# Kernel tuning notes

Measured on AMD Instinct MI355X. Metric: run time of the kernel, lower is better.

Reference implementation:

```python
import jax, jax.numpy as jnp
import numpy as np

NUM_USER = 24000
NUM_ITEM = 8000
DIM_E = 64
V_DIM = 2048
T_DIM = 384
TOPK = 10
N_UI_LAYERS = 2
LAMBDA = 0.9
N_INTER = 400000


def _build_sim(x):
    xn = x / jnp.linalg.norm(x, axis=-1, keepdims=True)
    return xn @ xn.T


def _knn_sym(sim, topk):
    # top-k per row -> sparse graph with symmetric (D^-1/2 A D^-1/2) normalization
    n = sim.shape[0]
    val, ind = jax.lax.top_k(sim, topk)            # [n, k]
    row = jnp.repeat(jnp.arange(n), topk)
    w = val.reshape(-1)
    col = ind.reshape(-1)
    deg = jax.ops.segment_sum(w, row, num_segments=n)
    dis = jnp.where(deg > 0, deg ** -0.5, 0.0)     # inf -> 0 as in torch masked_fill
    return col, dis[row] * w * dis[col]


def setup_inputs() -> dict:
    key = jax.random.key(0)
    ks = jax.random.split(key, 12)
    user_emb = jax.random.normal(ks[0], (NUM_USER, DIM_E), jnp.float32) * 0.1
    item_emb = jax.random.normal(ks[1], (NUM_ITEM, DIM_E), jnp.float32) * 0.1
    v_feat = jax.random.normal(ks[2], (NUM_ITEM, V_DIM), jnp.float32)
    t_feat = jax.random.normal(ks[3], (NUM_ITEM, T_DIM), jnp.float32)
    W_v = jax.random.normal(ks[4], (V_DIM, DIM_E), jnp.float32) * (1.0 / np.sqrt(V_DIM))
    b_v = jnp.zeros((DIM_E,), jnp.float32)
    W_t = jax.random.normal(ks[5], (T_DIM, DIM_E), jnp.float32) * (1.0 / np.sqrt(T_DIM))
    b_t = jnp.zeros((DIM_E,), jnp.float32)
    Wq1 = jax.random.normal(ks[6], (DIM_E, DIM_E), jnp.float32) * (1.0 / np.sqrt(DIM_E))
    bq1 = jnp.zeros((DIM_E,), jnp.float32)
    wq2 = jax.random.normal(ks[7], (DIM_E,), jnp.float32) * (1.0 / np.sqrt(DIM_E))
    # bipartite user-item interaction edges, symmetrized (as in __init__)
    u = jax.random.randint(ks[8], (N_INTER,), 0, NUM_USER)
    it = jax.random.randint(ks[9], (N_INTER,), 0, NUM_ITEM) + NUM_USER
    ei = jnp.stack([u, it])
    edge_index = jnp.concatenate([ei, ei[::-1]], axis=1)  # [2, 2*N_INTER]
    # original (frozen) multimodal KNN graphs built from raw features at init
    orig_img_cols, orig_img_w = _knn_sym(_build_sim(v_feat), TOPK)
    orig_txt_cols, orig_txt_w = _knn_sym(_build_sim(t_feat), TOPK)
    return {"user_emb": user_emb, "item_emb": item_emb, "v_feat": v_feat,
            "t_feat": t_feat, "W_v": W_v, "b_v": b_v, "W_t": W_t, "b_t": b_t,
            "Wq1": Wq1, "bq1": bq1, "wq2": wq2,
            "orig_img_w": orig_img_w, "orig_txt_w": orig_txt_w,
            "edge_index": edge_index,
            "orig_img_cols": orig_img_cols, "orig_txt_cols": orig_txt_cols}


def reference(user_emb, item_emb, v_feat, t_feat, W_v, b_v, W_t, b_t,
              Wq1, bq1, wq2, orig_img_w, orig_txt_w,
              edge_index, orig_img_cols, orig_txt_cols):
    n_user, n_item = user_emb.shape[0], item_emb.shape[0]
    # modality projections
    image_feats = v_feat @ W_v + b_v
    text_feats = t_feat @ W_t + b_t
    # fresh KNN graphs from projected features (build_item_graph=True path)
    img_cols, img_w = _knn_sym(_build_sim(image_feats), TOPK)
    txt_cols, txt_w = _knn_sym(_build_sim(text_feats), TOPK)
    row = jnp.repeat(jnp.arange(n_item), TOPK)

    def fused_spmm(cols_new, w_new, cols_orig, w_orig, x):
        # (1-lam)*A_new + lam*A_orig, applied as a single sparse matmul
        rows = jnp.concatenate([row, row])
        cols = jnp.concatenate([cols_new, cols_orig])
        w = jnp.concatenate([(1.0 - LAMBDA) * w_new,
                             LAMBDA * jax.lax.stop_gradient(w_orig)])
        return jax.ops.segment_sum(w[:, None] * x[cols], rows, num_segments=n_item)

    # NOTE: source bug reproduced - mm_layers loop always re-reads item_embedding,
    # so effective propagation depth is 1 regardless of mm_layers.
    image_item = fused_spmm(img_cols, img_w, orig_img_cols, orig_img_w, item_emb)
    text_item = fused_spmm(txt_cols, txt_w, orig_txt_cols, orig_txt_w, item_emb)

    def q(x):
        return jnp.tanh(x @ Wq1 + bq1) @ wq2  # [n_item]

    att = jnp.stack([q(image_item), q(text_item)], axis=-1)  # [n_item, 2]
    wgt = jax.nn.softmax(att, axis=-1)
    h = wgt[:, :1] * image_item + wgt[:, 1:] * text_item

    # user-item GCN propagation with sym degree normalization
    ego = jnp.concatenate([user_emb, item_emb], axis=0)
    n = ego.shape[0]
    r, c = edge_index[0], edge_index[1]
    deg = jax.ops.segment_sum(jnp.ones_like(r, dtype=ego.dtype), r, num_segments=n)
    dis = jnp.where(deg > 0, deg ** -0.5, 0.0)
    norm = dis[r] * dis[c]
    embs = [ego]
    for _ in range(N_UI_LAYERS):
        ego = jax.ops.segment_sum(norm[:, None] * ego[c], r, num_segments=n)
        embs.append(ego)
    all_emb = jnp.mean(jnp.stack(embs, axis=1), axis=1)
    u_g, i_g = all_emb[:n_user], all_emb[n_user:]
    h_norm = h / jnp.maximum(jnp.linalg.norm(h, axis=1, keepdims=True), 1e-12)
    i_g = i_g + h_norm
    return jnp.concatenate([u_g, i_g], axis=0)
```

## Files before the change

kernel.cpp:

```cpp
#include <hip/hip_runtime.h>
#include <math.h>

#define N_USER 24000
#define N_ITEM 8000
#define N_NODE 32000
#define N_EDGE 800000
#define NJC    16
#define JCH    512

typedef __attribute__((ext_vector_type(8))) short bf16x8;
typedef __attribute__((ext_vector_type(4))) float f32x4;

__device__ __forceinline__ float wred_sum(float v) {
#pragma unroll
  for (int off = 32; off; off >>= 1) v += __shfl_xor(v, off, 64);
  return v;
}

__device__ __forceinline__ unsigned short f2bf(float f) {
  unsigned int u = __float_as_uint(f);
  unsigned int r = (u + 0x7fffu + ((u >> 16) & 1u)) >> 16;
  return (unsigned short)r;
}
__device__ __forceinline__ float bf2f(unsigned short h) {
  return __uint_as_float(((unsigned int)h) << 16);
}

__device__ __forceinline__ unsigned int umx(unsigned int a, unsigned int b) { return a > b ? a : b; }
__device__ __forceinline__ unsigned int umn(unsigned int a, unsigned int b) { return a < b ? a : b; }

__device__ __forceinline__ float key_val(unsigned int k) {
  return ((float)(int)(k >> 13) - 131080.0f) * (1.0f / 131072.0f);
}
__device__ __forceinline__ int key_idx(unsigned int k) {
  return 8191 - (int)(k & 8191u);
}

#define ASTR 132
__global__ __launch_bounds__(256) void gemm_dual(
    const float* __restrict__ Xi, const float* __restrict__ Wi,
    const float* __restrict__ Xt, const float* __restrict__ Wt,
    float* __restrict__ Pi, float* __restrict__ Pt)
{
  __shared__ float As[32 * ASTR];
  __shared__ float Bs[32 * 64];
  const int tid = threadIdx.x;
  const int m0 = blockIdx.x * 128;
  const int cy = blockIdx.y;
  const float* X; const float* W; float* out; int K, kc0, Klen;
  if (cy < 8) { X = Xi; W = Wi; K = 2048; Klen = 256; kc0 = cy * 256;
                out = Pi + (size_t)cy * N_ITEM * 64; }
  else        { X = Xt; W = Wt; K = 384;  Klen = 128; kc0 = (cy - 8) * 128;
                out = Pt + (size_t)(cy - 8) * N_ITEM * 64; }
  const int tr = tid >> 4, tc = tid & 15;
  float acc[8][4] = {};
  for (int k0 = kc0; k0 < kc0 + Klen; k0 += 32) {
    __syncthreads();
#pragma unroll
    for (int lq = 0; lq < 4; ++lq) {
      int u = tid + lq * 256;
      int r = u >> 3, kq = u & 7;
      int row = m0 + r; if (row > N_ITEM - 1) row = N_ITEM - 1;
      float4 a = *(const float4*)(X + (size_t)row * K + k0 + kq * 4);
      As[(kq * 4 + 0) * ASTR + r] = a.x;
      As[(kq * 4 + 1) * ASTR + r] = a.y;
      As[(kq * 4 + 2) * ASTR + r] = a.z;
      As[(kq * 4 + 3) * ASTR + r] = a.w;
    }
#pragma unroll
    for (int lq = 0; lq < 2; ++lq) {
      int u = tid + lq * 256;
      int kb = u >> 4, nq = u & 15;
      *(float4*)(Bs + kb * 64 + nq * 4) =
          *(const float4*)(W + (size_t)(k0 + kb) * 64 + nq * 4);
    }
    __syncthreads();
#pragma unroll
    for (int k = 0; k < 32; ++k) {
      float4 a0 = *(const float4*)(As + k * ASTR + tr * 8);
      float4 a1 = *(const float4*)(As + k * ASTR + tr * 8 + 4);
      float4 b4 = *(const float4*)(Bs + k * 64 + tc * 4);
      float av[8] = {a0.x, a0.y, a0.z, a0.w, a1.x, a1.y, a1.z, a1.w};
      float bv[4] = {b4.x, b4.y, b4.z, b4.w};
#pragma unroll
      for (int ri = 0; ri < 8; ++ri)
#pragma unroll
        for (int ci = 0; ci < 4; ++ci) acc[ri][ci] += av[ri] * bv[ci];
    }
  }
#pragma unroll
  for (int ri = 0; ri < 8; ++ri) {
    int row = m0 + tr * 8 + ri;
    if (row < N_ITEM) {
      float4 o;
      o.x = acc[ri][0]; o.y = acc[ri][1]; o.z = acc[ri][2]; o.w = acc[ri][3];
      *(float4*)(out + (size_t)row * 64 + tc * 4) = o;
    }
  }
}

__global__ __launch_bounds__(256) void norm_dual(
    const float* __restrict__ Pi, const float* __restrict__ bi,
    unsigned short* __restrict__ Xhi, unsigned short* __restrict__ Xli,
    const float* __restrict__ Pt, const float* __restrict__ bt,
    unsigned short* __restrict__ Xht, unsigned short* __restrict__ Xlt)
{
  const float* P; const float* bias; unsigned short *Xh, *Xl; int nk;
  if (blockIdx.y == 0) { P = Pi; bias = bi; Xh = Xhi; Xl = Xli; nk = 8; }
  else                 { P = Pt; bias = bt; Xh = Xht; Xl = Xlt; nk = 3; }
  int row = blockIdx.x * 4 + (threadIdx.x >> 6);
  int lane = threadIdx.x & 63;
  size_t o = (size_t)row * 64 + lane;
  float v = bias[lane];
  for (int q = 0; q < nk; ++q) v += P[(size_t)q * N_ITEM * 64 + o];
  float ss = wred_sum(v * v);
  float xn = v * rsqrtf(ss);
  unsigned short hi = f2bf(xn);
  Xh[o] = hi;
  Xl[o] = f2bf(xn - bf2f(hi));
}

__global__ __launch_bounds__(256) void sim_topk_mfma(
    const unsigned short* __restrict__ Xhi, const unsigned short* __restrict__ Xli,
    const unsigned short* __restrict__ Xht, const unsigned short* __restrict__ Xlt,
    unsigned int* __restrict__ pk)
{
  __shared__ char lds[2 * 2 * 32 * 128];
  const unsigned short* Xh = blockIdx.z ? Xht : Xhi;
  const unsigned short* Xl = blockIdx.z ? Xlt : Xli;
  unsigned int* pkm = pk + (size_t)blockIdx.z * N_ITEM * (NJC * 10);

  const int tid = threadIdx.x;
  const int l = tid & 63;
  const int wid = tid >> 6;
  const int ib = blockIdx.x * 128 + wid * 32;
  const int jc = blockIdx.y * JCH;
  const bool lastc = (jc + JCH > N_ITEM);

  bf16x8 bh[2][2], bl[2][2];
#pragma unroll
  for (int s = 0; s < 2; ++s) {
    int irow = ib + s * 16 + (l & 15);
    if (irow > N_ITEM - 1) irow = N_ITEM - 1;
    int ksl = (l >> 4) * 8;
#pragma unroll
    for (int kh = 0; kh < 2; ++kh) {
      bh[s][kh] = *(const bf16x8*)(Xh + (size_t)irow * 64 + kh * 32 + ksl);
      bl[s][kh] = *(const bf16x8*)(Xl + (size_t)irow * 64 + kh * 32 + ksl);
    }
  }

  unsigned int K0[10], K1[10];
#pragma unroll
  for (int t = 0; t < 10; ++t) { K0[t] = 0u; K1[t] = 0u; }

  auto stage = [&](int b, int p) {
    int row = tid >> 3, cb = (tid & 7) * 16;
    int gr = jc + p * 32 + row;
    if (gr > N_ITEM - 1) gr = N_ITEM - 1;
    int4 vh = *(const int4*)(Xh + (size_t)gr * 64 + (cb >> 1));
    int4 vl = *(const int4*)(Xl + (size_t)gr * 64 + (cb >> 1));
    int bo = (row * 128 + cb) ^ ((row & 7) << 4);
    *(int4*)(lds + b * 8192 + bo) = vh;
    *(int4*)(lds + b * 8192 + 4096 + bo) = vl;
  };

#define EPI(MASKED)                                                            \
  _Pragma("unroll")                                                            \
  for (int s = 0; s < 2; ++s) {                                                \
    unsigned int* K = s ? K1 : K0;                                             \
    _Pragma("unroll")                                                          \
    for (int t = 0; t < 2; ++t) {                                              \
      _Pragma("unroll")                                                        \
      for (int r = 0; r < 4; ++r) {                                            \
        float f = acc[t][s][r];                                                \
        unsigned int v19 = (unsigned int)(int)(f * 131072.0f + 131080.0f);     \
        unsigned int key = (v19 << 13) | (unsigned int)jinv[t * 4 + r];        \
        if (MASKED) key = (jinv[t * 4 + r] >= 192) ? key : 0u;                 \
        _Pragma("unroll")                                                      \
        for (int q = 0; q < 10; ++q) {                                         \
          unsigned int mn = umn(K[q], key);                                    \
          K[q] = umx(K[q], key);                                               \
          key = mn;                                                            \
        }                                                                      \
      }                                                                        \
    }                                                                          \
  }

  stage(0, 0);
  int cur = 0;
  for (int p = 0; p < 16; ++p) {
    __syncthreads();
    if (p < 15) stage(cur ^ 1, p + 1);
    const char* ldsH = lds + cur * 8192;
    const char* ldsL = ldsH + 4096;
    f32x4 acc[2][2] = {};
#pragma unroll
    for (int t = 0; t < 2; ++t) {
      int jr = t * 16 + (l & 15);
      int sw = (jr & 7) << 4;
      int rb = jr * 128 + ((l >> 4) << 4);
      bf16x8 ah0 = *(const bf16x8*)(ldsH + (rb ^ sw));
      bf16x8 ah1 = *(const bf16x8*)(ldsH + ((rb + 64) ^ sw));
      bf16x8 al0 = *(const bf16x8*)(ldsL + (rb ^ sw));
      bf16x8 al1 = *(const bf16x8*)(ldsL + ((rb + 64) ^ sw));
#pragma unroll
      for (int s = 0; s < 2; ++s) {
        acc[t][s] = __builtin_amdgcn_mfma_f32_16x16x32_bf16(ah0, bh[s][0], acc[t][s], 0, 0, 0);
        acc[t][s] = __builtin_amdgcn_mfma_f32_16x16x32_bf16(ah1, bh[s][1], acc[t][s], 0, 0, 0);
        acc[t][s] = __builtin_amdgcn_mfma_f32_16x16x32_bf16(ah0, bl[s][0], acc[t][s], 0, 0, 0);
        acc[t][s] = __builtin_amdgcn_mfma_f32_16x16x32_bf16(ah1, bl[s][1], acc[t][s], 0, 0, 0);
        acc[t][s] = __builtin_amdgcn_mfma_f32_16x16x32_bf16(al0, bh[s][0], acc[t][s], 0, 0, 0);
        acc[t][s] = __builtin_amdgcn_mfma_f32_16x16x32_bf16(al1, bh[s][1], acc[t][s], 0, 0, 0);
      }
    }
    const int jg0 = jc + p * 32 + ((l >> 4) << 2);
    int jinv[8];
#pragma unroll
    for (int t = 0; t < 2; ++t)
#pragma unroll
      for (int r = 0; r < 4; ++r)
        jinv[t * 4 + r] = 8191 - (jg0 + t * 16 + r);
    if (!lastc) { EPI(false) } else { EPI(true) }
    cur ^= 1;
  }
#undef EPI

#pragma unroll
  for (int s = 0; s < 2; ++s) {
    unsigned int* K = s ? K1 : K0;
    unsigned int kv[10];
#pragma unroll
    for (int t = 0; t < 10; ++t) {
      unsigned int m = K[0];
      m = umx(m, (unsigned int)__shfl_xor((int)m, 16, 64));
      m = umx(m, (unsigned int)__shfl_xor((int)m, 32, 64));
      bool own = (K[0] == m);
#pragma unroll
      for (int q2 = 0; q2 < 9; ++q2) K[q2] = own ? K[q2 + 1] : K[q2];
      K[9] = own ? 0u : K[9];
      kv[t] = m;
    }
    int i = ib + s * 16 + (l & 15);
    if (l < 16 && i < N_ITEM) {
      size_t base = ((size_t)i * NJC + blockIdx.y) * 10;
#pragma unroll
      for (int t = 0; t < 10; ++t) pkm[base + t] = kv[t];
    }
  }
}

__global__ __launch_bounds__(256) void merge_topk(
    const unsigned int* __restrict__ pk,
    float* __restrict__ tv_i, int* __restrict__ tc_i, float* __restrict__ dis_i,
    float* __restrict__ tv_t, int* __restrict__ tc_t, float* __restrict__ dis_t)
{
  float* tv; int* tc; float* dis;
  if (blockIdx.y == 0) { tv = tv_i; tc = tc_i; dis = dis_i; }
  else                 { tv = tv_t; tc = tc_t; dis = dis_t; }
  int lane = threadIdx.x & 63;
  int row = blockIdx.x * 4 + (threadIdx.x >> 6);
  size_t base = (size_t)blockIdx.y * N_ITEM * (NJC * 10) + (size_t)row * (NJC * 10);
  unsigned int k0 = pk[base + lane];
  unsigned int k1 = pk[base + 64 + lane];
  unsigned int k2 = (lane < 32) ? pk[base + 128 + lane] : 0u;
  float deg = 0.f, keepv = 0.f; int keepc = 0;
  for (int t = 0; t < 10; ++t) {
    unsigned int m = umx(umx(k0, k1), k2);
#pragma unroll
    for (int off = 32; off; off >>= 1)
      m = umx(m, (unsigned int)__shfl_xor((int)m, off, 64));
    deg += key_val(m);
    if (k0 == m) k0 = 0u;
    else if (k1 == m) k1 = 0u;
    else if (k2 == m) k2 = 0u;
    if (lane == t) { keepv = key_val(m); keepc = key_idx(m); }
  }
  if (lane < 10) { tv[(size_t)row * 10 + lane] = keepv; tc[(size_t)row * 10 + lane] = keepc; }
  if (lane == 0) dis[row] = deg > 0.f ? rsqrtf(deg) : 0.f;
}

__global__ __launch_bounds__(256) void spmm_attn(
    const float* __restrict__ tv_i, const int* __restrict__ tc_i, const float* __restrict__ dis_i,
    const float* __restrict__ ow_i, const int* __restrict__ oc_i,
    const float* __restrict__ tv_t, const int* __restrict__ tc_t, const float* __restrict__ dis_t,
    const float* __restrict__ ow_t, const int* __restrict__ oc_t,
    const float* __restrict__ item_emb,
    const float* __restrict__ Wq1, const float* __restrict__ bq1,
    const float* __restrict__ wq2, float* __restrict__ hn)
{
  __shared__ float Wlds[64 * 64];
  __shared__ float sm[4][2][64];
  int tid = threadIdx.x;
  int lane = tid & 63, wid = tid >> 6;
  int row = blockIdx.x * 4 + wid;
#pragma unroll
  for (int s = 0; s < 4; ++s) {
    int idx = tid + s * 256;
    ((float4*)Wlds)[idx] = ((const float4*)Wq1)[idx];
  }
  float a0 = 0.f, a1 = 0.f;
  {
    float disr = dis_i[row];
#pragma unroll
    for (int t = 0; t < 10; ++t) {
      int c = tc_i[(size_t)row * 10 + t];
      a0 += 0.1f * disr * tv_i[(size_t)row * 10 + t] * dis_i[c] * item_emb[(size_t)c * 64 + lane];
    }
#pragma unroll
    for (int t = 0; t < 10; ++t) {
      int c = oc_i[(size_t)row * 10 + t];
      a0 += 0.9f * ow_i[(size_t)row * 10 + t] * item_emb[(size_t)c * 64 + lane];
    }
  }
  {
    float disr = dis_t[row];
#pragma unroll
    for (int t = 0; t < 10; ++t) {
      int c = tc_t[(size_t)row * 10 + t];
      a1 += 0.1f * disr * tv_t[(size_t)row * 10 + t] * dis_t[c] * item_emb[(size_t)c * 64 + lane];
    }
#pragma unroll
    for (int t = 0; t < 10; ++t) {
      int c = oc_t[(size_t)row * 10 + t];
      a1 += 0.9f * ow_t[(size_t)row * 10 + t] * item_emb[(size_t)c * 64 + lane];
    }
  }
  sm[wid][0][lane] = a0;
  sm[wid][1][lane] = a1;
  __syncthreads();
  float y0 = bq1[lane], y1 = bq1[lane];
  for (int k = 0; k < 64; ++k) {
    float w = Wlds[k * 64 + lane];
    y0 += sm[wid][0][k] * w;
    y1 += sm[wid][1][k] * w;
  }
  float wq = wq2[lane];
  float s0 = wred_sum(tanhf(y0) * wq);
  float s1 = wred_sum(tanhf(y1) * wq);
  float mx = fmaxf(s0, s1);
  float e0 = expf(s0 - mx), e1 = expf(s1 - mx);
  float inv = 1.f / (e0 + e1);
  float h = (e0 * inv) * a0 + (e1 * inv) * a1;
  float n2 = wred_sum(h * h);
  float nrm = fmaxf(sqrtf(n2), 1e-12f);
  hn[(size_t)row * 64 + lane] = h / nrm;
}

__global__ void ui_zero(int* degi, int* cursor)
{
  int n = blockIdx.x * 256 + threadIdx.x;
  if (n < N_NODE) { degi[n] = 0; cursor[n] = 0; }
}

__global__ void ui_count(const int* __restrict__ r, int* degi)
{
  int e = blockIdx.x * 256 + threadIdx.x;
  if (e < N_EDGE) atomicAdd(&degi[r[e]], 1);
}

__global__ __launch_bounds__(256) void ui_blocksum(const int* __restrict__ degi, int* __restrict__ bsum)
{
  __shared__ int ws4[4];
  int tid = threadIdx.x;
  int v = degi[blockIdx.x * 256 + tid];
#pragma unroll
  for (int off = 32; off; off >>= 1) v += __shfl_xor(v, off, 64);
  if ((tid & 63) == 0) ws4[tid >> 6] = v;
  __syncthreads();
  if (tid == 0) bsum[blockIdx.x] = ws4[0] + ws4[1] + ws4[2] + ws4[3];
}

__global__ __launch_bounds__(128) void ui_scanb(const int* __restrict__ bsum, int* __restrict__ bbase, int* __restrict__ offs)
{
  __shared__ int s[128];
  int t = threadIdx.x;
  int v = (t < 125) ? bsum[t] : 0;
  s[t] = v;
  __syncthreads();
  for (int off = 1; off < 128; off <<= 1) {
    int tmp = (t >= off) ? s[t - off] : 0;
    __syncthreads();
    s[t] += tmp;
    __syncthreads();
  }
  if (t < 125) bbase[t] = s[t] - v;
  if (t == 127) offs[N_NODE] = s[127];
}

__global__ __launch_bounds__(256) void ui_scanc(const int* __restrict__ degi, const int* __restrict__ bbase,
                                                int* __restrict__ offs, float* __restrict__ disui)
{
  __shared__ int wt[4];
  int tid = threadIdx.x;
  int i = blockIdx.x * 256 + tid;
  int d = degi[i];
  int v = d;
#pragma unroll
  for (int off = 1; off < 64; off <<= 1) {
    int n = __shfl_up(v, off, 64);
    if ((tid & 63) >= off) v += n;
  }
  if ((tid & 63) == 63) wt[tid >> 6] = v;
  __syncthreads();
  int add = bbase[blockIdx.x];
  for (int w = 0; w < (tid >> 6); ++w) add += wt[w];
  offs[i] = add + v - d;
  disui[i] = d > 0 ? rsqrtf((float)d) : 0.f;
}

__global__ void ui_fill(const int* __restrict__ r, const int* __restrict__ c,
                        const int* __restrict__ offs, int* cursor, int* __restrict__ csr)
{
  int e = blockIdx.x * 256 + threadIdx.x;
  if (e < N_EDGE) {
    int rr = r[e];
    int pos = offs[rr] + atomicAdd(&cursor[rr], 1);
    csr[pos] = c[e];
  }
}

template <bool FIRST, bool FINAL>
__global__ __launch_bounds__(256) void ui_prop(
    const float* __restrict__ in, const float* __restrict__ ue,
    const float* __restrict__ ie, float* __restrict__ out,
    const int* __restrict__ offs, const int* __restrict__ csr,
    const float* __restrict__ dis, const float* __restrict__ hn)
{
  int tid = threadIdx.x;
  int lane = tid & 63, wid = tid >> 6;
  int row = blockIdx.x * 4 + wid;
  int q = lane >> 3, c8 = lane & 7;
  float4 acc0 = make_float4(0.f, 0.f, 0.f, 0.f);
  float4 acc1 = make_float4(0.f, 0.f, 0.f, 0.f);
  int e0 = offs[row], e1 = offs[row + 1];
  for (int e = e0 + q; e < e1; e += 8) {
    int cc = csr[e];
    const float* src = FIRST
        ? (cc < N_USER ? ue + (size_t)cc * 64 : ie + (size_t)(cc - N_USER) * 64)
        : in + (size_t)cc * 64;
    float4 v0 = *(const float4*)(src + c8 * 8);
    float4 v1 = *(const float4*)(src + c8 * 8 + 4);
    float d = dis[cc];
    acc0.x += d * v0.x; acc0.y += d * v0.y; acc0.z += d * v0.z; acc0.w += d * v0.w;
    acc1.x += d * v1.x; acc1.y += d * v1.y; acc1.z += d * v1.z; acc1.w += d * v1.w;
  }
#pragma unroll
  for (int off = 8; off <= 32; off <<= 1) {
    acc0.x += __shfl_xor(acc0.x, off, 64);
    acc0.y += __shfl_xor(acc0.y, off, 64);
    acc0.z += __shfl_xor(acc0.z, off, 64);
    acc0.w += __shfl_xor(acc0.w, off, 64);
    acc1.x += __shfl_xor(acc1.x, off, 64);
    acc1.y += __shfl_xor(acc1.y, off, 64);
    acc1.z += __shfl_xor(acc1.z, off, 64);
    acc1.w += __shfl_xor(acc1.w, off, 64);
  }
  if (q == 0) {
    float dr = dis[row];
    acc0.x *= dr; acc0.y *= dr; acc0.z *= dr; acc0.w *= dr;
    acc1.x *= dr; acc1.y *= dr; acc1.z *= dr; acc1.w *= dr;
    if (!FINAL) {
      *(float4*)(out + (size_t)row * 64 + c8 * 8) = acc0;
      *(float4*)(out + (size_t)row * 64 + c8 * 8 + 4) = acc1;
    } else {
      const float* egop = (row < N_USER) ? ue + (size_t)row * 64
                                         : ie + (size_t)(row - N_USER) * 64;
      float4 eg0 = *(const float4*)(egop + c8 * 8);
      float4 eg1 = *(const float4*)(egop + c8 * 8 + 4);
      float4 l10 = *(const float4*)(in + (size_t)row * 64 + c8 * 8);
      float4 l11 = *(const float4*)(in + (size_t)row * 64 + c8 * 8 + 4);
      float4 o0, o1;
      o0.x = (eg0.x + l10.x + acc0.x) * (1.f / 3.f);
      o0.y = (eg0.y + l10.y + acc0.y) * (1.f / 3.f);
      o0.z = (eg0.z + l10.z + acc0.z) * (1.f / 3.f);
      o0.w = (eg0.w + l10.w + acc0.w) * (1.f / 3.f);
      o1.x = (eg1.x + l11.x + acc1.x) * (1.f / 3.f);
      o1.y = (eg1.y + l11.y + acc1.y) * (1.f / 3.f);
      o1.z = (eg1.z + l11.z + acc1.z) * (1.f / 3.f);
      o1.w = (eg1.w + l11.w + acc1.w) * (1.f / 3.f);
      if (row >= N_USER) {
        const float* hp = hn + (size_t)(row - N_USER) * 64;
        float4 h0 = *(const float4*)(hp + c8 * 8);
        float4 h1 = *(const float4*)(hp + c8 * 8 + 4);
        o0.x += h0.x; o0.y += h0.y; o0.z += h0.z; o0.w += h0.w;
        o1.x += h1.x; o1.y += h1.y; o1.z += h1.z; o1.w += h1.w;
      }
      *(float4*)(out + (size_t)row * 64 + c8 * 8) = o0;
      *(float4*)(out + (size_t)row * 64 + c8 * 8 + 4) = o1;
    }
  }
}

extern "C" void kernel_launch(void* const* d_in, const int* in_sizes, int n_in,
                              void* d_out, int out_size, void* d_ws, size_t ws_size,
                              hipStream_t stream)
{
  (void)in_sizes; (void)n_in; (void)out_size; (void)ws_size;
  const float* user_emb = (const float*)d_in[0];
  const float* item_emb = (const float*)d_in[1];
  const float* v_feat   = (const float*)d_in[2];
  const float* t_feat   = (const float*)d_in[3];
  const float* W_v      = (const float*)d_in[4];
  const float* b_v      = (const float*)d_in[5];
  const float* W_t      = (const float*)d_in[6];
  const float* b_t      = (const float*)d_in[7];
  const float* Wq1      = (const float*)d_in[8];
  const float* bq1      = (const float*)d_in[9];
  const float* wq2      = (const float*)d_in[10];
  const float* ow_i     = (const float*)d_in[11];
  const float* ow_t     = (const float*)d_in[12];
  const int*   eidx     = (const int*)d_in[13];
  const int*   oc_i     = (const int*)d_in[14];
  const int*   oc_t     = (const int*)d_in[15];
  float* out = (float*)d_out;

  char* wp = (char*)d_ws;
  auto alloc = [&](size_t bytes) -> void* {
    void* p = (void*)wp;
    wp += (bytes + 255) & ~(size_t)255;
    return p;
  };
  char* regionA = (char*)alloc((size_t)8 * N_ITEM * 64 * 4 + 1024);
  char* regionB = (char*)alloc((size_t)N_NODE * 64 * 4 + 1024);
  float* Pp_i = (float*)regionA;
  float* Pp_t = (float*)regionB;
  unsigned int* pk = (unsigned int*)regionA;
  float* E1 = (float*)regionB;

  unsigned short* Xhi = (unsigned short*)alloc((size_t)N_ITEM * 64 * 2);
  unsigned short* Xli = (unsigned short*)alloc((size_t)N_ITEM * 64 * 2);
  unsigned short* Xht = (unsigned short*)alloc((size_t)N_ITEM * 64 * 2);
  unsigned short* Xlt = (unsigned short*)alloc((size_t)N_ITEM * 64 * 2);
  float* tv_i  = (float*)alloc((size_t)N_ITEM * 10 * 4);
  int*   tc_i  = (int*)  alloc((size_t)N_ITEM * 10 * 4);
  float* dis_i = (float*)alloc((size_t)N_ITEM * 4);
  float* tv_t  = (float*)alloc((size_t)N_ITEM * 10 * 4);
  int*   tc_t  = (int*)  alloc((size_t)N_ITEM * 10 * 4);
  float* dis_t = (float*)alloc((size_t)N_ITEM * 4);
  float* hn    = (float*)alloc((size_t)N_ITEM * 64 * 4);
  int*   degi  = (int*)  alloc((size_t)N_NODE * 4);
  int*   curs  = (int*)  alloc((size_t)N_NODE * 4);
  int*   offs  = (int*)  alloc((size_t)(N_NODE + 1) * 4);
  float* disui = (float*)alloc((size_t)N_NODE * 4);
  int*   csr   = (int*)  alloc((size_t)N_EDGE * 4);
  int*   bsum  = (int*)  alloc((size_t)128 * 4);
  int*   bbase = (int*)  alloc((size_t)128 * 4);

  gemm_dual<<<dim3(63, 11), 256, 0, stream>>>(v_feat, W_v, t_feat, W_t, Pp_i, Pp_t);
  norm_dual<<<dim3(2000, 2), 256, 0, stream>>>(Pp_i, b_v, Xhi, Xli, Pp_t, b_t, Xht, Xlt);
  sim_topk_mfma<<<dim3(63, NJC, 2), 256, 0, stream>>>(Xhi, Xli, Xht, Xlt, pk);
  merge_topk<<<dim3(2000, 2), 256, 0, stream>>>(pk, tv_i, tc_i, dis_i, tv_t, tc_t, dis_t);
  spmm_attn<<<2000, 256, 0, stream>>>(tv_i, tc_i, dis_i, ow_i, oc_i,
                                      tv_t, tc_t, dis_t, ow_t, oc_t,
                                      item_emb, Wq1, bq1, wq2, hn);
  ui_zero<<<125, 256, 0, stream>>>(degi, curs);
  ui_count<<<N_EDGE / 256, 256, 0, stream>>>(eidx, degi);
  ui_blocksum<<<125, 256, 0, stream>>>(degi, bsum);
  ui_scanb<<<1, 128, 0, stream>>>(bsum, bbase, offs);
  ui_scanc<<<125, 256, 0, stream>>>(degi, bbase, offs, disui);
  ui_fill<<<N_EDGE / 256, 256, 0, stream>>>(eidx, eidx + N_EDGE, offs, curs, csr);
  ui_prop<true, false><<<8000, 256, 0, stream>>>(nullptr, user_emb, item_emb, E1, offs, csr, disui, nullptr);
  ui_prop<false, true><<<8000, 256, 0, stream>>>(E1, user_emb, item_emb, out, offs, csr, disui, hn);
}
```

Baseline: 308.3 us.

## Fuse UI graph build stages into multimodal kernels to cut launch count

The independent user-item CSR construction steps (degree count, scan, fill, first propagation) are piggybacked onto the multimodal pipeline kernels as extra blocks, selected by block index. Kernel launches drop from 13 to 6, and the two pipelines can overlap inside each launch. The three-kernel scan becomes one single-block serial scan, and the zeroing kernel becomes a memset. The price is a serial 125-iteration scan in one block, which may end up on the critical path, and heterogeneous blocks sharing a grid.

```diff
diff --git a/kernel.cpp b/kernel.cpp
--- a/kernel.cpp
+++ b/kernel.cpp
@@ -37,16 +37,24 @@
 }
 
 #define ASTR 132
-__global__ __launch_bounds__(256) void gemm_dual(
+#define NB_G 693
+__global__ __launch_bounds__(256) void k_gemm_count(
     const float* __restrict__ Xi, const float* __restrict__ Wi,
     const float* __restrict__ Xt, const float* __restrict__ Wt,
-    float* __restrict__ Pi, float* __restrict__ Pt)
+    float* __restrict__ Pi, float* __restrict__ Pt,
+    const int* __restrict__ r, int* __restrict__ degi)
 {
   __shared__ float As[32 * ASTR];
   __shared__ float Bs[32 * 64];
   const int tid = threadIdx.x;
-  const int m0 = blockIdx.x * 128;
-  const int cy = blockIdx.y;
+  const int b = blockIdx.x;
+  if (b >= NB_G) {
+    int e = (b - NB_G) * 256 + tid;
+    atomicAdd(&degi[r[e]], 1);
+    return;
+  }
+  const int m0 = (b % 63) * 128;
+  const int cy = b / 63;
   const float* X; const float* W; float* out; int K, kc0, Klen;
   if (cy < 8) { X = Xi; W = Wi; K = 2048; Klen = 256; kc0 = cy * 256;
                 out = Pi + (size_t)cy * N_ITEM * 64; }
@@ -59,13 +67,13 @@
 #pragma unroll
     for (int lq = 0; lq < 4; ++lq) {
       int u = tid + lq * 256;
-      int r = u >> 3, kq = u & 7;
-      int row = m0 + r; if (row > N_ITEM - 1) row = N_ITEM - 1;
+      int rr = u >> 3, kq = u & 7;
+      int row = m0 + rr; if (row > N_ITEM - 1) row = N_ITEM - 1;
       float4 a = *(const float4*)(X + (size_t)row * K + k0 + kq * 4);
-      As[(kq * 4 + 0) * ASTR + r] = a.x;
-      As[(kq * 4 + 1) * ASTR + r] = a.y;
-      As[(kq * 4 + 2) * ASTR + r] = a.z;
-      As[(kq * 4 + 3) * ASTR + r] = a.w;
+      As[(kq * 4 + 0) * ASTR + rr] = a.x;
+      As[(kq * 4 + 1) * ASTR + rr] = a.y;
+      As[(kq * 4 + 2) * ASTR + rr] = a.z;
+      As[(kq * 4 + 3) * ASTR + rr] = a.w;
     }
 #pragma unroll
     for (int lq = 0; lq < 2; ++lq) {
@@ -120,21 +128,55 @@
   Xl[o] = f2bf(xn - bf2f(hi));
 }
 
-__global__ __launch_bounds__(256) void sim_topk_mfma(
+#define NB_SIM 2016
+__global__ __launch_bounds__(256) void k_sim_scan(
     const unsigned short* __restrict__ Xhi, const unsigned short* __restrict__ Xli,
     const unsigned short* __restrict__ Xht, const unsigned short* __restrict__ Xlt,
-    unsigned int* __restrict__ pk)
+    unsigned int* __restrict__ pk,
+    const int* __restrict__ degi, int* __restrict__ offs, float* __restrict__ disui)
 {
   __shared__ char lds[2 * 2 * 32 * 128];
-  const unsigned short* Xh = blockIdx.z ? Xht : Xhi;
-  const unsigned short* Xl = blockIdx.z ? Xlt : Xli;
-  unsigned int* pkm = pk + (size_t)blockIdx.z * N_ITEM * (NJC * 10);
-
+  __shared__ int wsum[4];
   const int tid = threadIdx.x;
+
+  if (blockIdx.x == NB_SIM) {
+    int lane = tid & 63, wid = tid >> 6;
+    int running = 0;
+    for (int k = 0; k < 125; ++k) {
+      int i = k * 256 + tid;
+      int d = degi[i];
+      int v = d;
+#pragma unroll
+      for (int off = 1; off < 64; off <<= 1) {
+        int n = __shfl_up(v, off, 64);
+        if (lane >= off) v += n;
+      }
+      if (lane == 63) wsum[wid] = v;
+      __syncthreads();
+      int add = running;
+      for (int w = 0; w < wid; ++w) add += wsum[w];
+      offs[i] = add + v - d;
+      disui[i] = d > 0 ? rsqrtf((float)d) : 0.f;
+      int tot = wsum[0] + wsum[1] + wsum[2] + wsum[3];
+      __syncthreads();
+      running += tot;
+    }
+    if (tid == 0) offs[N_NODE] = running;
+    return;
+  }
+
+  const int bz = blockIdx.x / 1008;
+  const int rem = blockIdx.x % 1008;
+  const int by = rem / 63;
+  const int bx = rem % 63;
+  const unsigned short* Xh = bz ? Xht : Xhi;
+  const unsigned short* Xl = bz ? Xlt : Xli;
+  unsigned int* pkm = pk + (size_t)bz * N_ITEM * (NJC * 10);
+
   const int l = tid & 63;
   const int wid = tid >> 6;
-  const int ib = blockIdx.x * 128 + wid * 32;
-  const int jc = blockIdx.y * JCH;
+  const int ib = bx * 128 + wid * 32;
+  const int jc = by * JCH;
   const bool lastc = (jc + JCH > N_ITEM);
 
   bf16x8 bh[2][2], bl[2][2];
@@ -243,24 +285,37 @@
     }
     int i = ib + s * 16 + (l & 15);
     if (l < 16 && i < N_ITEM) {
-      size_t base = ((size_t)i * NJC + blockIdx.y) * 10;
+      size_t base = ((size_t)i * NJC + by) * 10;
 #pragma unroll
       for (int t = 0; t < 10; ++t) pkm[base + t] = kv[t];
     }
   }
 }
 
-__global__ __launch_bounds__(256) void merge_topk(
+#define NB_M 4000
+__global__ __launch_bounds__(256) void k_merge_fill(
     const unsigned int* __restrict__ pk,
     float* __restrict__ tv_i, int* __restrict__ tc_i, float* __restrict__ dis_i,
-    float* __restrict__ tv_t, int* __restrict__ tc_t, float* __restrict__ dis_t)
-{
+    float* __restrict__ tv_t, int* __restrict__ tc_t, float* __restrict__ dis_t,
+    const int* __restrict__ r, const int* __restrict__ c,
+    const int* __restrict__ offs, int* __restrict__ cursor, int* __restrict__ csr)
+{
+  int b = blockIdx.x;
+  int tid = threadIdx.x;
+  if (b >= NB_M) {
+    int e = (b - NB_M) * 256 + tid;
+    int rr = r[e];
+    int pos = offs[rr] + atomicAdd(&cursor[rr], 1);
+    csr[pos] = c[e];
+    return;
+  }
+  int my = b / 2000, mx = b % 2000;
   float* tv; int* tc; float* dis;
-  if (blockIdx.y == 0) { tv = tv_i; tc = tc_i; dis = dis_i; }
-  else                 { tv = tv_t; tc = tc_t; dis = dis_t; }
-  int lane = threadIdx.x & 63;
-  int row = blockIdx.x * 4 + (threadIdx.x >> 6);
-  size_t base = (size_t)blockIdx.y * N_ITEM * (NJC * 10) + (size_t)row * (NJC * 10);
+  if (my == 0) { tv = tv_i; tc = tc_i; dis = dis_i; }
+  else         { tv = tv_t; tc = tc_t; dis = dis_t; }
+  int lane = tid & 63;
+  int row = mx * 4 + (tid >> 6);
+  size_t base = (size_t)my * N_ITEM * (NJC * 10) + (size_t)row * (NJC * 10);
   unsigned int k0 = pk[base + lane];
   unsigned int k1 = pk[base + 64 + lane];
   unsigned int k2 = (lane < 32) ? pk[base + 128 + lane] : 0u;
@@ -280,20 +335,61 @@
   if (lane == 0) dis[row] = deg > 0.f ? rsqrtf(deg) : 0.f;
 }
 
-__global__ __launch_bounds__(256) void spmm_attn(
+#define NB_S 2000
+__global__ __launch_bounds__(256) void k_spmm_prop1(
     const float* __restrict__ tv_i, const int* __restrict__ tc_i, const float* __restrict__ dis_i,
     const float* __restrict__ ow_i, const int* __restrict__ oc_i,
     const float* __restrict__ tv_t, const int* __restrict__ tc_t, const float* __restrict__ dis_t,
     const float* __restrict__ ow_t, const int* __restrict__ oc_t,
     const float* __restrict__ item_emb,
     const float* __restrict__ Wq1, const float* __restrict__ bq1,
-    const float* __restrict__ wq2, float* __restrict__ hn)
+    const float* __restrict__ wq2, float* __restrict__ hn,
+    const float* __restrict__ ue, float* __restrict__ E1,
+    const int* __restrict__ offs, const int* __restrict__ csr,
+    const float* __restrict__ dis)
 {
   __shared__ float Wlds[64 * 64];
   __shared__ float sm[4][2][64];
   int tid = threadIdx.x;
   int lane = tid & 63, wid = tid >> 6;
-  int row = blockIdx.x * 4 + wid;
+  int b = blockIdx.x;
+  if (b >= NB_S) {
+    int row = (b - NB_S) * 4 + wid;
+    int q = lane >> 3, c8 = lane & 7;
+    float4 acc0 = make_float4(0.f, 0.f, 0.f, 0.f);
+    float4 acc1 = make_float4(0.f, 0.f, 0.f, 0.f);
+    int e0 = offs[row], e1 = offs[row + 1];
+    for (int e = e0 + q; e < e1; e += 8) {
+      int cc = csr[e];
+      const float* src = cc < N_USER ? ue + (size_t)cc * 64
+                                     : item_emb + (size_t)(cc - N_USER) * 64;
+      float4 v0 = *(const float4*)(src + c8 * 8);
+      float4 v1 = *(const float4*)(src + c8 * 8 + 4);
+      float d = dis[cc];
+      acc0.x += d * v0.x; acc0.y += d * v0.y; acc0.z += d * v0.z; acc0.w += d * v0.w;
+      acc1.x += d * v1.x; acc1.y += d * v1.y; acc1.z += d * v1.z; acc1.w += d * v1.w;
+    }
+#pragma unroll
+    for (int off = 8; off <= 32; off <<= 1) {
+      acc0.x += __shfl_xor(acc0.x, off, 64);
+      acc0.y += __shfl_xor(acc0.y, off, 64);
+      acc0.z += __shfl_xor(acc0.z, off, 64);
+      acc0.w += __shfl_xor(acc0.w, off, 64);
+      acc1.x += __shfl_xor(acc1.x, off, 64);
+      acc1.y += __shfl_xor(acc1.y, off, 64);
+      acc1.z += __shfl_xor(acc1.z, off, 64);
+      acc1.w += __shfl_xor(acc1.w, off, 64);
+    }
+    if (q == 0) {
+      float dr = dis[row];
+      acc0.x *= dr; acc0.y *= dr; acc0.z *= dr; acc0.w *= dr;
+      acc1.x *= dr; acc1.y *= dr; acc1.z *= dr; acc1.w *= dr;
+      *(float4*)(E1 + (size_t)row * 64 + c8 * 8) = acc0;
+      *(float4*)(E1 + (size_t)row * 64 + c8 * 8 + 4) = acc1;
+    }
+    return;
+  }
+  int row = b * 4 + wid;
 #pragma unroll
   for (int s = 0; s < 4; ++s) {
     int idx = tid + s * 256;
@@ -347,81 +443,7 @@
   hn[(size_t)row * 64 + lane] = h / nrm;
 }
 
-__global__ void ui_zero(int* degi, int* cursor)
-{
-  int n = blockIdx.x * 256 + threadIdx.x;
-  if (n < N_NODE) { degi[n] = 0; cursor[n] = 0; }
-}
-
-__global__ void ui_count(const int* __restrict__ r, int* degi)
-{
-  int e = blockIdx.x * 256 + threadIdx.x;
-  if (e < N_EDGE) atomicAdd(&degi[r[e]], 1);
-}
-
-__global__ __launch_bounds__(256) void ui_blocksum(const int* __restrict__ degi, int* __restrict__ bsum)
-{
-  __shared__ int ws4[4];
-  int tid = threadIdx.x;
-  int v = degi[blockIdx.x * 256 + tid];
-#pragma unroll
-  for (int off = 32; off; off >>= 1) v += __shfl_xor(v, off, 64);
-  if ((tid & 63) == 0) ws4[tid >> 6] = v;
-  __syncthreads();
-  if (tid == 0) bsum[blockIdx.x] = ws4[0] + ws4[1] + ws4[2] + ws4[3];
-}
-
-__global__ __launch_bounds__(128) void ui_scanb(const int* __restrict__ bsum, int* __restrict__ bbase, int* __restrict__ offs)
-{
-  __shared__ int s[128];
-  int t = threadIdx.x;
-  int v = (t < 125) ? bsum[t] : 0;
-  s[t] = v;
-  __syncthreads();
-  for (int off = 1; off < 128; off <<= 1) {
-    int tmp = (t >= off) ? s[t - off] : 0;
-    __syncthreads();
-    s[t] += tmp;
-    __syncthreads();
-  }
-  if (t < 125) bbase[t] = s[t] - v;
-  if (t == 127) offs[N_NODE] = s[127];
-}
-
-__global__ __launch_bounds__(256) void ui_scanc(const int* __restrict__ degi, const int* __restrict__ bbase,
-                                                int* __restrict__ offs, float* __restrict__ disui)
-{
-  __shared__ int wt[4];
-  int tid = threadIdx.x;
-  int i = blockIdx.x * 256 + tid;
-  int d = degi[i];
-  int v = d;
-#pragma unroll
-  for (int off = 1; off < 64; off <<= 1) {
-    int n = __shfl_up(v, off, 64);
-    if ((tid & 63) >= off) v += n;
-  }
-  if ((tid & 63) == 63) wt[tid >> 6] = v;
-  __syncthreads();
-  int add = bbase[blockIdx.x];
-  for (int w = 0; w < (tid >> 6); ++w) add += wt[w];
-  offs[i] = add + v - d;
-  disui[i] = d > 0 ? rsqrtf((float)d) : 0.f;
-}
-
-__global__ void ui_fill(const int* __restrict__ r, const int* __restrict__ c,
-                        const int* __restrict__ offs, int* cursor, int* __restrict__ csr)
-{
-  int e = blockIdx.x * 256 + threadIdx.x;
-  if (e < N_EDGE) {
-    int rr = r[e];
-    int pos = offs[rr] + atomicAdd(&cursor[rr], 1);
-    csr[pos] = c[e];
-  }
-}
-
-template <bool FIRST, bool FINAL>
-__global__ __launch_bounds__(256) void ui_prop(
+__global__ __launch_bounds__(256) void k_prop2(
     const float* __restrict__ in, const float* __restrict__ ue,
     const float* __restrict__ ie, float* __restrict__ out,
     const int* __restrict__ offs, const int* __restrict__ csr,
@@ -436,9 +458,7 @@
   int e0 = offs[row], e1 = offs[row + 1];
   for (int e = e0 + q; e < e1; e += 8) {
     int cc = csr[e];
-    const float* src = FIRST
-        ? (cc < N_USER ? ue + (size_t)cc * 64 : ie + (size_t)(cc - N_USER) * 64)
-        : in + (size_t)cc * 64;
+    const float* src = in + (size_t)cc * 64;
     float4 v0 = *(const float4*)(src + c8 * 8);
     float4 v1 = *(const float4*)(src + c8 * 8 + 4);
     float d = dis[cc];
@@ -460,35 +480,30 @@
     float dr = dis[row];
     acc0.x *= dr; acc0.y *= dr; acc0.z *= dr; acc0.w *= dr;
     acc1.x *= dr; acc1.y *= dr; acc1.z *= dr; acc1.w *= dr;
-    if (!FINAL) {
-      *(float4*)(out + (size_t)row * 64 + c8 * 8) = acc0;
-      *(float4*)(out + (size_t)row * 64 + c8 * 8 + 4) = acc1;
-    } else {
-      const float* egop = (row < N_USER) ? ue + (size_t)row * 64
-                                         : ie + (size_t)(row - N_USER) * 64;
-      float4 eg0 = *(const float4*)(egop + c8 * 8);
-      float4 eg1 = *(const float4*)(egop + c8 * 8 + 4);
-      float4 l10 = *(const float4*)(in + (size_t)row * 64 + c8 * 8);
-      float4 l11 = *(const float4*)(in + (size_t)row * 64 + c8 * 8 + 4);
-      float4 o0, o1;
-      o0.x = (eg0.x + l10.x + acc0.x) * (1.f / 3.f);
-      o0.y = (eg0.y + l10.y + acc0.y) * (1.f / 3.f);
-      o0.z = (eg0.z + l10.z + acc0.z) * (1.f / 3.f);
-      o0.w = (eg0.w + l10.w + acc0.w) * (1.f / 3.f);
-      o1.x = (eg1.x + l11.x + acc1.x) * (1.f / 3.f);
-      o1.y = (eg1.y + l11.y + acc1.y) * (1.f / 3.f);
-      o1.z = (eg1.z + l11.z + acc1.z) * (1.f / 3.f);
-      o1.w = (eg1.w + l11.w + acc1.w) * (1.f / 3.f);
-      if (row >= N_USER) {
-        const float* hp = hn + (size_t)(row - N_USER) * 64;
-        float4 h0 = *(const float4*)(hp + c8 * 8);
-        float4 h1 = *(const float4*)(hp + c8 * 8 + 4);
-        o0.x += h0.x; o0.y += h0.y; o0.z += h0.z; o0.w += h0.w;
-        o1.x += h1.x; o1.y += h1.y; o1.z += h1.z; o1.w += h1.w;
-      }
-      *(float4*)(out + (size_t)row * 64 + c8 * 8) = o0;
-      *(float4*)(out + (size_t)row * 64 + c8 * 8 + 4) = o1;
-    }
+    const float* egop = (row < N_USER) ? ue + (size_t)row * 64
+                                       : ie + (size_t)(row - N_USER) * 64;
+    float4 eg0 = *(const float4*)(egop + c8 * 8);
+    float4 eg1 = *(const float4*)(egop + c8 * 8 + 4);
+    float4 l10 = *(const float4*)(in + (size_t)row * 64 + c8 * 8);
+    float4 l11 = *(const float4*)(in + (size_t)row * 64 + c8 * 8 + 4);
+    float4 o0, o1;
+    o0.x = (eg0.x + l10.x + acc0.x) * (1.f / 3.f);
+    o0.y = (eg0.y + l10.y + acc0.y) * (1.f / 3.f);
+    o0.z = (eg0.z + l10.z + acc0.z) * (1.f / 3.f);
+    o0.w = (eg0.w + l10.w + acc0.w) * (1.f / 3.f);
+    o1.x = (eg1.x + l11.x + acc1.x) * (1.f / 3.f);
+    o1.y = (eg1.y + l11.y + acc1.y) * (1.f / 3.f);
+    o1.z = (eg1.z + l11.z + acc1.z) * (1.f / 3.f);
+    o1.w = (eg1.w + l11.w + acc1.w) * (1.f / 3.f);
+    if (row >= N_USER) {
+      const float* hp = hn + (size_t)(row - N_USER) * 64;
+      float4 h0 = *(const float4*)(hp + c8 * 8);
+      float4 h1 = *(const float4*)(hp + c8 * 8 + 4);
+      o0.x += h0.x; o0.y += h0.y; o0.z += h0.z; o0.w += h0.w;
+      o1.x += h1.x; o1.y += h1.y; o1.z += h1.z; o1.w += h1.w;
+    }
+    *(float4*)(out + (size_t)row * 64 + c8 * 8) = o0;
+    *(float4*)(out + (size_t)row * 64 + c8 * 8 + 4) = o1;
   }
 }
 
@@ -539,27 +554,23 @@
   int*   tc_t  = (int*)  alloc((size_t)N_ITEM * 10 * 4);
   float* dis_t = (float*)alloc((size_t)N_ITEM * 4);
   float* hn    = (float*)alloc((size_t)N_ITEM * 64 * 4);
-  int*   degi  = (int*)  alloc((size_t)N_NODE * 4);
-  int*   curs  = (int*)  alloc((size_t)N_NODE * 4);
+  int*   degcur= (int*)  alloc((size_t)2 * N_NODE * 4);
+  int*   degi  = degcur;
+  int*   curs  = degcur + N_NODE;
   int*   offs  = (int*)  alloc((size_t)(N_NODE + 1) * 4);
   float* disui = (float*)alloc((size_t)N_NODE * 4);
   int*   csr   = (int*)  alloc((size_t)N_EDGE * 4);
-  int*   bsum  = (int*)  alloc((size_t)128 * 4);
-  int*   bbase = (int*)  alloc((size_t)128 * 4);
-
-  gemm_dual<<<dim3(63, 11), 256, 0, stream>>>(v_feat, W_v, t_feat, W_t, Pp_i, Pp_t);
+
+  hipMemsetAsync(degcur, 0, (size_t)2 * N_NODE * 4, stream);
+  k_gemm_count<<<NB_G + 3125, 256, 0, stream>>>(v_feat, W_v, t_feat, W_t, Pp_i, Pp_t,
+                                                eidx, degi);
   norm_dual<<<dim3(2000, 2), 256, 0, stream>>>(Pp_i, b_v, Xhi, Xli, Pp_t, b_t, Xht, Xlt);
-  sim_topk_mfma<<<dim3(63, NJC, 2), 256, 0, stream>>>(Xhi, Xli, Xht, Xlt, pk);
-  merge_topk<<<dim3(2000, 2), 256, 0, stream>>>(pk, tv_i, tc_i, dis_i, tv_t, tc_t, dis_t);
-  spmm_attn<<<2000, 256, 0, stream>>>(tv_i, tc_i, dis_i, ow_i, oc_i,
-                                      tv_t, tc_t, dis_t, ow_t, oc_t,
-                                      item_emb, Wq1, bq1, wq2, hn);
-  ui_zero<<<125, 256, 0, stream>>>(degi, curs);
-  ui_count<<<N_EDGE / 256, 256, 0, stream>>>(eidx, degi);
-  ui_blocksum<<<125, 256, 0, stream>>>(degi, bsum);
-  ui_scanb<<<1, 128, 0, stream>>>(bsum, bbase, offs);
-  ui_scanc<<<125, 256, 0, stream>>>(degi, bbase, offs, disui);
-  ui_fill<<<N_EDGE / 256, 256, 0, stream>>>(eidx, eidx + N_EDGE, offs, curs, csr);
-  ui_prop<true, false><<<8000, 256, 0, stream>>>(nullptr, user_emb, item_emb, E1, offs, csr, disui, nullptr);
-  ui_prop<false, true><<<8000, 256, 0, stream>>>(E1, user_emb, item_emb, out, offs, csr, disui, hn);
-}
+  k_sim_scan<<<NB_SIM + 1, 256, 0, stream>>>(Xhi, Xli, Xht, Xlt, pk, degi, offs, disui);
+  k_merge_fill<<<NB_M + 3125, 256, 0, stream>>>(pk, tv_i, tc_i, dis_i, tv_t, tc_t, dis_t,
+                                                eidx, eidx + N_EDGE, offs, curs, csr);
+  k_spmm_prop1<<<NB_S + 8000, 256, 0, stream>>>(tv_i, tc_i, dis_i, ow_i, oc_i,
+                                                tv_t, tc_t, dis_t, ow_t, oc_t,
+                                                item_emb, Wq1, bq1, wq2, hn,
+                                                user_emb, E1, offs, csr, disui);
+  k_prop2<<<8000, 256, 0, stream>>>(E1, user_emb, item_emb, out, offs, csr, disui, hn);
+}
```

Result: slower. 353.0 us (+14.5%).
